# Optimization experiments

Hardware: AMD Instinct MI355X
Metric: run time of the kernel (lower is better)

The kernel has to match this reference:

```python
import jax, jax.numpy as jnp
import numpy as np

MAX_LEN = 128
N_SYMBOLS = 32000
HIDDEN = 1024
BATCH = 32


def setup_inputs() -> dict:
    key = jax.random.key(0)
    ks = jax.random.split(key, 8)
    s = 0.05  # weight scale for numerical stability
    return {
        "h": jax.random.normal(ks[0], (BATCH, HIDDEN), jnp.float32),
        "w_ih": jax.random.normal(ks[1], (3 * HIDDEN, HIDDEN), jnp.float32) * s,
        "w_hh": jax.random.normal(ks[2], (3 * HIDDEN, HIDDEN), jnp.float32) * s,
        "b_ih": jax.random.normal(ks[3], (3 * HIDDEN,), jnp.float32) * s,
        "b_hh": jax.random.normal(ks[4], (3 * HIDDEN,), jnp.float32) * s,
        "cls_w": jax.random.normal(ks[5], (N_SYMBOLS, HIDDEN), jnp.float32) * s,
        "cls_b": jax.random.normal(ks[6], (N_SYMBOLS,), jnp.float32) * s,
        "emb": jax.random.normal(ks[7], (N_SYMBOLS + 1, HIDDEN), jnp.float32),
    }


def reference(h, w_ih, w_hh, b_ih, b_hh, cls_w, cls_b, emb):
    B = h.shape[0]
    # BOS token embedding (row n_symbols), broadcast over batch.
    x0 = jnp.broadcast_to(emb[N_SYMBOLS], (B, HIDDEN))

    def step(carry, _):
        x, hs = carry
        gi = x @ w_ih.T + b_ih      # [B, 3H]
        gh = hs @ w_hh.T + b_hh     # [B, 3H]
        i_r, i_z, i_n = jnp.split(gi, 3, axis=-1)
        h_r, h_z, h_n = jnp.split(gh, 3, axis=-1)
        r = jax.nn.sigmoid(i_r + h_r)
        z = jax.nn.sigmoid(i_z + h_z)
        n = jnp.tanh(i_n + r * h_n)
        h_new = (1.0 - z) * n + z * hs
        logits = h_new @ cls_w.T + cls_b            # [B, V]
        tok = jnp.argmax(logits, axis=-1)            # [B]
        x_new = emb[tok]                             # [B, H]
        return (x_new, h_new), logits

    (_, _), logits = jax.lax.scan(step, (x0, h), None, length=MAX_LEN)
    # [max_len, B, n_symbols] == torch's cat(dim=-2).transpose(0, 1)
    return logits
```

## Files before the change

kernel.cpp:

```cpp
#include <hip/hip_runtime.h>
#include <math.h>

#define MAX_LEN 128
#define NSYM    32000
#define HID     1024
#define BATCH   32


__device__ __forceinline__ unsigned fkey(float x) {
    unsigned u = __float_as_uint(x);
    return (u & 0x80000000u) ? ~u : (u | 0x80000000u);
}

__global__ void init_slots(unsigned long long* slots) {
    int i = blockIdx.x * blockDim.x + threadIdx.x;
    if (i < MAX_LEN * BATCH) slots[i] = 0ULL;
}

__global__ __launch_bounds__(256) void gru_step(
    const float* __restrict__ h_in,
    const float* __restrict__ w_ih,
    const float* __restrict__ w_hh,
    const float* __restrict__ b_ih,
    const float* __restrict__ b_hh,
    const float* __restrict__ emb,
    const float* __restrict__ h_prev,
    float* __restrict__ h_next,
    const unsigned long long* __restrict__ slot_prev,
    int t)
{
    __shared__ float a_t[2][BATCH][129];
    __shared__ float w_t[24][128];
    __shared__ float s_gh[128][3];
    __shared__ int   s_tok[BATCH];

    const int tid  = threadIdx.x;
    const int pair = tid & 127;
    const int half = tid >> 7;
    const int b    = pair & 31;
    const int jj   = pair >> 5;
    const int j0   = blockIdx.x * 4;

    if (tid < BATCH) {
        int tok;
        if (t == 0) tok = NSYM;
        else {
            unsigned long long s = slot_prev[tid];
            tok = (int)(0xFFFFFFFFu - (unsigned)(s & 0xFFFFFFFFull));
        }
        s_tok[tid] = tok;
    }
    __syncthreads();

    const float* hp = (t == 0) ? h_in : h_prev;

    float acc0 = 0.f, acc1 = 0.f, acc2 = 0.f;

    float4 pw[3], pa[8];

    {
        const int k0 = 0;
        #pragma unroll
        for (int i = 0; i < 3; ++i) {
            int f = tid + 256 * i;
            int r = f >> 5, kq = f & 31;
            int rh = r / 12, rem = r % 12, g = rem >> 2, jx = rem & 3;
            const float* wsrc = rh ? w_hh : w_ih;
            size_t row = (size_t)(j0 + jx + 1024 * g);
            pw[i] = *(const float4*)&wsrc[row * HID + k0 + 4 * kq];
        }
        #pragma unroll
        for (int i = 0; i < 8; ++i) {
            int f = tid + 256 * i;
            int hh = f >> 10, bb = (f >> 5) & 31, kq = f & 31;
            const float* src = (hh == 0) ? &emb[(size_t)s_tok[bb] * HID]
                                         : &hp[(size_t)bb * HID];
            pa[i] = *(const float4*)&src[k0 + 4 * kq];
        }
    }

    const float* ar = &a_t[half][b][0];
    const float* w0 = &w_t[half * 12 + 0 + jj][0];
    const float* w1 = &w_t[half * 12 + 4 + jj][0];
    const float* w2 = &w_t[half * 12 + 8 + jj][0];

    for (int c = 0; c < 8; ++c) {
        __syncthreads();
        #pragma unroll
        for (int i = 0; i < 3; ++i) {
            int f = tid + 256 * i;
            int r = f >> 5, kq = f & 31;
            *(float4*)&w_t[r][4 * kq] = pw[i];
        }
        #pragma unroll
        for (int i = 0; i < 8; ++i) {
            int f = tid + 256 * i;
            int hh = f >> 10, bb = (f >> 5) & 31, kq = f & 31;
            float* dst = &a_t[hh][bb][4 * kq];
            dst[0] = pa[i].x; dst[1] = pa[i].y; dst[2] = pa[i].z; dst[3] = pa[i].w;
        }
        __syncthreads();

        if (c + 1 < 8) {
            const int k0 = (c + 1) * 128;
            #pragma unroll
            for (int i = 0; i < 3; ++i) {
                int f = tid + 256 * i;
                int r = f >> 5, kq = f & 31;
                int rh = r / 12, rem = r % 12, g = rem >> 2, jx = rem & 3;
                const float* wsrc = rh ? w_hh : w_ih;
                size_t row = (size_t)(j0 + jx + 1024 * g);
                pw[i] = *(const float4*)&wsrc[row * HID + k0 + 4 * kq];
            }
            #pragma unroll
            for (int i = 0; i < 8; ++i) {
                int f = tid + 256 * i;
                int hh = f >> 10, bb = (f >> 5) & 31, kq = f & 31;
                const float* src = (hh == 0) ? &emb[(size_t)s_tok[bb] * HID]
                                             : &hp[(size_t)bb * HID];
                pa[i] = *(const float4*)&src[k0 + 4 * kq];
            }
        }

        #pragma unroll 16
        for (int kk = 0; kk < 128; ++kk) {
            float av = ar[kk];
            acc0 = fmaf(av, w0[kk], acc0);
            acc1 = fmaf(av, w1[kk], acc1);
            acc2 = fmaf(av, w2[kk], acc2);
        }
    }

    __syncthreads();
    if (half == 1) {
        s_gh[pair][0] = acc0; s_gh[pair][1] = acc1; s_gh[pair][2] = acc2;
    }
    __syncthreads();
    if (half == 0) {
        int j = j0 + jj;
        float gir = acc0 + b_ih[j];
        float giz = acc1 + b_ih[j + 1024];
        float gin = acc2 + b_ih[j + 2048];
        float ghr = s_gh[pair][0] + b_hh[j];
        float ghz = s_gh[pair][1] + b_hh[j + 1024];
        float ghn = s_gh[pair][2] + b_hh[j + 2048];
        float r = 1.f / (1.f + expf(-(gir + ghr)));
        float z = 1.f / (1.f + expf(-(giz + ghz)));
        float n = tanhf(gin + r * ghn);
        float hv = hp[(size_t)b * HID + j];
        h_next[(size_t)b * HID + j] = (1.f - z) * n + z * hv;
    }
}

__global__ __launch_bounds__(256) void cls_step(
    const float* __restrict__ h_cur,
    const float* __restrict__ cls_w,
    const float* __restrict__ cls_b,
    float* __restrict__ out_t,
    unsigned long long* __restrict__ slot_t)
{
    __shared__ float w_t[128][65];
    __shared__ float a_t[BATCH][65];
    __shared__ unsigned long long s_best[BATCH];

    const int tid = threadIdx.x;
    const int tx  = tid & 31;
    const int ty  = tid >> 5;
    const int v0  = blockIdx.x * 128;

    if (tid < BATCH) s_best[tid] = 0ULL;

    float acc[4][4];
    #pragma unroll
    for (int i = 0; i < 4; ++i)
        #pragma unroll
        for (int m = 0; m < 4; ++m) acc[i][m] = 0.f;

    float4 pw[8], pa[2];

    {
        const int k0 = 0;
        #pragma unroll
        for (int i = 0; i < 8; ++i) {
            int f = tid + 256 * i;
            int v = f >> 4, kq = f & 15;
            pw[i] = *(const float4*)&cls_w[(size_t)(v0 + v) * HID + k0 + 4 * kq];
        }
        #pragma unroll
        for (int i = 0; i < 2; ++i) {
            int f = tid + 256 * i;
            int bb = f >> 4, kq = f & 15;
            pa[i] = *(const float4*)&h_cur[(size_t)bb * HID + k0 + 4 * kq];
        }
    }

    for (int c = 0; c < 16; ++c) {
        __syncthreads();
        #pragma unroll
        for (int i = 0; i < 8; ++i) {
            int f = tid + 256 * i;
            int v = f >> 4, kq = f & 15;
            float* dst = &w_t[v][4 * kq];
            dst[0] = pw[i].x; dst[1] = pw[i].y; dst[2] = pw[i].z; dst[3] = pw[i].w;
        }
        #pragma unroll
        for (int i = 0; i < 2; ++i) {
            int f = tid + 256 * i;
            int bb = f >> 4, kq = f & 15;
            float* dst = &a_t[bb][4 * kq];
            dst[0] = pa[i].x; dst[1] = pa[i].y; dst[2] = pa[i].z; dst[3] = pa[i].w;
        }
        __syncthreads();

        if (c + 1 < 16) {
            const int k0 = (c + 1) * 64;
            #pragma unroll
            for (int i = 0; i < 8; ++i) {
                int f = tid + 256 * i;
                int v = f >> 4, kq = f & 15;
                pw[i] = *(const float4*)&cls_w[(size_t)(v0 + v) * HID + k0 + 4 * kq];
            }
            #pragma unroll
            for (int i = 0; i < 2; ++i) {
                int f = tid + 256 * i;
                int bb = f >> 4, kq = f & 15;
                pa[i] = *(const float4*)&h_cur[(size_t)bb * HID + k0 + 4 * kq];
            }
        }

        #pragma unroll 8
        for (int kk = 0; kk < 64; ++kk) {
            float av[4], wv[4];
            #pragma unroll
            for (int i = 0; i < 4; ++i) av[i] = a_t[4 * ty + i][kk];
            #pragma unroll
            for (int m = 0; m < 4; ++m) wv[m] = w_t[tx + 32 * m][kk];
            #pragma unroll
            for (int i = 0; i < 4; ++i)
                #pragma unroll
                for (int m = 0; m < 4; ++m)
                    acc[i][m] = fmaf(av[i], wv[m], acc[i][m]);
        }
    }

    float cb[4];
    #pragma unroll
    for (int m = 0; m < 4; ++m) cb[m] = cls_b[v0 + tx + 32 * m];

    #pragma unroll
    for (int i = 0; i < 4; ++i) {
        int b = 4 * ty + i;
        unsigned long long best = 0ULL;
        #pragma unroll
        for (int m = 0; m < 4; ++m) {
            int v = v0 + tx + 32 * m;
            float val = acc[i][m] + cb[m];
            out_t[(size_t)b * NSYM + v] = val;
            unsigned long long pk =
                ((unsigned long long)fkey(val) << 32) |
                (unsigned long long)(0xFFFFFFFFu - (unsigned)v);
            if (pk > best) best = pk;
        }
        atomicMax(&s_best[b], best);
    }
    __syncthreads();
    if (tid < BATCH) atomicMax(&slot_t[tid], s_best[tid]);
}

extern "C" void kernel_launch(void* const* d_in, const int* in_sizes, int n_in,
                              void* d_out, int out_size, void* d_ws, size_t ws_size,
                              hipStream_t stream) {
    const float* h0    = (const float*)d_in[0];
    const float* w_ih  = (const float*)d_in[1];
    const float* w_hh  = (const float*)d_in[2];
    const float* b_ih  = (const float*)d_in[3];
    const float* b_hh  = (const float*)d_in[4];
    const float* cls_w = (const float*)d_in[5];
    const float* cls_b = (const float*)d_in[6];
    const float* emb   = (const float*)d_in[7];
    float* out = (float*)d_out;

    float* h_buf = (float*)d_ws;
    unsigned long long* slots =
        (unsigned long long*)((char*)d_ws + (size_t)2 * BATCH * HID * sizeof(float));

    init_slots<<<16, 256, 0, stream>>>(slots);

    for (int t = 0; t < MAX_LEN; ++t) {
        float* h_prev = h_buf + (size_t)((t + 1) & 1) * BATCH * HID;
        float* h_next = h_buf + (size_t)(t & 1) * BATCH * HID;
        const unsigned long long* slot_prev = slots + (size_t)(t > 0 ? (t - 1) : 0) * BATCH;

        gru_step<<<256, 256, 0, stream>>>(h0, w_ih, w_hh, b_ih, b_hh, emb,
                                          h_prev, h_next, slot_prev, t);
        cls_step<<<250, 256, 0, stream>>>(h_next, cls_w, cls_b,
                                          out + (size_t)t * BATCH * NSYM,
                                          slots + (size_t)t * BATCH);
    }
}
```

Measured before the change: 13.25 ms.

## Swizzle LDS tiles for float4 reads and stage logits for coalesced stores

Both GRU and classifier kernels replace padded shared-memory tiles with XOR-swizzled layouts, so inner loops can use float4 LDS reads without bank conflicts. The classifier thread mapping changes to a 2x8 register tile, and logits are transposed through shared memory so global stores go out as coalesced float4 writes. Launch bounds add a minimum of one block per CU. The aim is fewer LDS instructions, fewer bank conflicts and wider output stores. The cost is extra syncs and a shared-memory transpose in the epilogue.

```diff
diff --git a/kernel.cpp b/kernel.cpp
--- a/kernel.cpp
+++ b/kernel.cpp
@@ -17,7 +17,7 @@
     if (i < MAX_LEN * BATCH) slots[i] = 0ULL;
 }
 
-__global__ __launch_bounds__(256) void gru_step(
+__global__ __launch_bounds__(256, 1) void gru_step(
     const float* __restrict__ h_in,
     const float* __restrict__ w_ih,
     const float* __restrict__ w_hh,
@@ -29,24 +29,23 @@
     const unsigned long long* __restrict__ slot_prev,
     int t)
 {
-    __shared__ float a_t[2][BATCH][129];
     __shared__ float w_t[24][128];
+    __shared__ float a_t[2][32][128];
     __shared__ float s_gh[128][3];
     __shared__ int   s_tok[BATCH];
 
-    const int tid  = threadIdx.x;
-    const int pair = tid & 127;
-    const int half = tid >> 7;
-    const int b    = pair & 31;
-    const int jj   = pair >> 5;
-    const int j0   = blockIdx.x * 4;
+    const int tid = threadIdx.x;
+    const int b   = tid & 31;
+    const int j   = (tid >> 5) & 3;
+    const int s   = tid >> 7;
+    const int j0  = blockIdx.x * 4;
 
     if (tid < BATCH) {
         int tok;
         if (t == 0) tok = NSYM;
         else {
-            unsigned long long s = slot_prev[tid];
-            tok = (int)(0xFFFFFFFFu - (unsigned)(s & 0xFFFFFFFFull));
+            unsigned long long sl = slot_prev[tid];
+            tok = (int)(0xFFFFFFFFu - (unsigned)(sl & 0xFFFFFFFFull));
         }
         s_tok[tid] = tok;
     }
@@ -55,7 +54,6 @@
     const float* hp = (t == 0) ? h_in : h_prev;
 
     float acc0 = 0.f, acc1 = 0.f, acc2 = 0.f;
-
     float4 pw[3], pa[8];
 
     {
@@ -64,25 +62,24 @@
         for (int i = 0; i < 3; ++i) {
             int f = tid + 256 * i;
             int r = f >> 5, kq = f & 31;
-            int rh = r / 12, rem = r % 12, g = rem >> 2, jx = rem & 3;
-            const float* wsrc = rh ? w_hh : w_ih;
-            size_t row = (size_t)(j0 + jx + 1024 * g);
-            pw[i] = *(const float4*)&wsrc[row * HID + k0 + 4 * kq];
+            int rs = r / 12, rem = r % 12, g = rem >> 2, jx = rem & 3;
+            const float* wsrc = rs ? w_hh : w_ih;
+            pw[i] = *(const float4*)&wsrc[(size_t)(j0 + jx + 1024 * g) * HID + k0 + 4 * kq];
         }
         #pragma unroll
         for (int i = 0; i < 8; ++i) {
             int f = tid + 256 * i;
-            int hh = f >> 10, bb = (f >> 5) & 31, kq = f & 31;
-            const float* src = (hh == 0) ? &emb[(size_t)s_tok[bb] * HID]
-                                         : &hp[(size_t)bb * HID];
+            int ss = f >> 10, bb = (f >> 5) & 31, kq = f & 31;
+            const float* src = ss ? &hp[(size_t)bb * HID]
+                                  : &emb[(size_t)s_tok[bb] * HID];
             pa[i] = *(const float4*)&src[k0 + 4 * kq];
         }
     }
 
-    const float* ar = &a_t[half][b][0];
-    const float* w0 = &w_t[half * 12 + 0 + jj][0];
-    const float* w1 = &w_t[half * 12 + 4 + jj][0];
-    const float* w2 = &w_t[half * 12 + 8 + jj][0];
+    const float* wr0 = &w_t[12 * s + 0 + j][0];
+    const float* wr1 = &w_t[12 * s + 4 + j][0];
+    const float* wr2 = &w_t[12 * s + 8 + j][0];
+    const float* arow = &a_t[s][b][0];
 
     for (int c = 0; c < 8; ++c) {
         __syncthreads();
@@ -95,9 +92,8 @@
         #pragma unroll
         for (int i = 0; i < 8; ++i) {
             int f = tid + 256 * i;
-            int hh = f >> 10, bb = (f >> 5) & 31, kq = f & 31;
-            float* dst = &a_t[hh][bb][4 * kq];
-            dst[0] = pa[i].x; dst[1] = pa[i].y; dst[2] = pa[i].z; dst[3] = pa[i].w;
+            int ss = f >> 10, bb = (f >> 5) & 31, kq = f & 31;
+            *(float4*)&a_t[ss][bb][4 * (kq ^ bb)] = pa[i];
         }
         __syncthreads();
 
@@ -107,74 +103,81 @@
             for (int i = 0; i < 3; ++i) {
                 int f = tid + 256 * i;
                 int r = f >> 5, kq = f & 31;
-                int rh = r / 12, rem = r % 12, g = rem >> 2, jx = rem & 3;
-                const float* wsrc = rh ? w_hh : w_ih;
-                size_t row = (size_t)(j0 + jx + 1024 * g);
-                pw[i] = *(const float4*)&wsrc[row * HID + k0 + 4 * kq];
+                int rs = r / 12, rem = r % 12, g = rem >> 2, jx = rem & 3;
+                const float* wsrc = rs ? w_hh : w_ih;
+                pw[i] = *(const float4*)&wsrc[(size_t)(j0 + jx + 1024 * g) * HID + k0 + 4 * kq];
             }
             #pragma unroll
             for (int i = 0; i < 8; ++i) {
                 int f = tid + 256 * i;
-                int hh = f >> 10, bb = (f >> 5) & 31, kq = f & 31;
-                const float* src = (hh == 0) ? &emb[(size_t)s_tok[bb] * HID]
-                                             : &hp[(size_t)bb * HID];
+                int ss = f >> 10, bb = (f >> 5) & 31, kq = f & 31;
+                const float* src = ss ? &hp[(size_t)bb * HID]
+                                      : &emb[(size_t)s_tok[bb] * HID];
                 pa[i] = *(const float4*)&src[k0 + 4 * kq];
             }
         }
 
-        #pragma unroll 16
-        for (int kk = 0; kk < 128; ++kk) {
-            float av = ar[kk];
-            acc0 = fmaf(av, w0[kk], acc0);
-            acc1 = fmaf(av, w1[kk], acc1);
-            acc2 = fmaf(av, w2[kk], acc2);
-        }
-    }
-
-    __syncthreads();
-    if (half == 1) {
+        #pragma unroll 8
+        for (int q = 0; q < 32; ++q) {
+            float4 av = *(const float4*)&arow[4 * (q ^ b)];
+            float4 w0 = *(const float4*)&wr0[4 * q];
+            float4 w1 = *(const float4*)&wr1[4 * q];
+            float4 w2 = *(const float4*)&wr2[4 * q];
+            acc0 = fmaf(av.x, w0.x, acc0); acc0 = fmaf(av.y, w0.y, acc0);
+            acc0 = fmaf(av.z, w0.z, acc0); acc0 = fmaf(av.w, w0.w, acc0);
+            acc1 = fmaf(av.x, w1.x, acc1); acc1 = fmaf(av.y, w1.y, acc1);
+            acc1 = fmaf(av.z, w1.z, acc1); acc1 = fmaf(av.w, w1.w, acc1);
+            acc2 = fmaf(av.x, w2.x, acc2); acc2 = fmaf(av.y, w2.y, acc2);
+            acc2 = fmaf(av.z, w2.z, acc2); acc2 = fmaf(av.w, w2.w, acc2);
+        }
+    }
+
+    __syncthreads();
+    if (s == 1) {
+        int pair = tid & 127;
         s_gh[pair][0] = acc0; s_gh[pair][1] = acc1; s_gh[pair][2] = acc2;
     }
     __syncthreads();
-    if (half == 0) {
-        int j = j0 + jj;
-        float gir = acc0 + b_ih[j];
-        float giz = acc1 + b_ih[j + 1024];
-        float gin = acc2 + b_ih[j + 2048];
-        float ghr = s_gh[pair][0] + b_hh[j];
-        float ghz = s_gh[pair][1] + b_hh[j + 1024];
-        float ghn = s_gh[pair][2] + b_hh[j + 2048];
+    if (s == 0) {
+        int pair = tid & 127;
+        int jg = j0 + j;
+        float gir = acc0 + b_ih[jg];
+        float giz = acc1 + b_ih[jg + 1024];
+        float gin = acc2 + b_ih[jg + 2048];
+        float ghr = s_gh[pair][0] + b_hh[jg];
+        float ghz = s_gh[pair][1] + b_hh[jg + 1024];
+        float ghn = s_gh[pair][2] + b_hh[jg + 2048];
         float r = 1.f / (1.f + expf(-(gir + ghr)));
         float z = 1.f / (1.f + expf(-(giz + ghz)));
         float n = tanhf(gin + r * ghn);
-        float hv = hp[(size_t)b * HID + j];
-        h_next[(size_t)b * HID + j] = (1.f - z) * n + z * hv;
-    }
-}
-
-__global__ __launch_bounds__(256) void cls_step(
+        float hv = hp[(size_t)b * HID + jg];
+        h_next[(size_t)b * HID + jg] = (1.f - z) * n + z * hv;
+    }
+}
+
+__global__ __launch_bounds__(256, 1) void cls_step(
     const float* __restrict__ h_cur,
     const float* __restrict__ cls_w,
     const float* __restrict__ cls_b,
     float* __restrict__ out_t,
     unsigned long long* __restrict__ slot_t)
 {
-    __shared__ float w_t[128][65];
-    __shared__ float a_t[BATCH][65];
+    __shared__ float w_t[128][64];
+    __shared__ float a_t[32][64];
     __shared__ unsigned long long s_best[BATCH];
 
     const int tid = threadIdx.x;
-    const int tx  = tid & 31;
-    const int ty  = tid >> 5;
+    const int bq  = tid & 15;
+    const int vg  = tid >> 4;
     const int v0  = blockIdx.x * 128;
 
     if (tid < BATCH) s_best[tid] = 0ULL;
 
-    float acc[4][4];
+    float acc[2][8];
     #pragma unroll
-    for (int i = 0; i < 4; ++i)
-        #pragma unroll
-        for (int m = 0; m < 4; ++m) acc[i][m] = 0.f;
+    for (int h = 0; h < 2; ++h)
+        #pragma unroll
+        for (int i = 0; i < 8; ++i) acc[h][i] = 0.f;
 
     float4 pw[8], pa[2];
 
@@ -200,15 +203,13 @@
         for (int i = 0; i < 8; ++i) {
             int f = tid + 256 * i;
             int v = f >> 4, kq = f & 15;
-            float* dst = &w_t[v][4 * kq];
-            dst[0] = pw[i].x; dst[1] = pw[i].y; dst[2] = pw[i].z; dst[3] = pw[i].w;
+            *(float4*)&w_t[v][4 * (kq ^ (v & 15))] = pw[i];
         }
         #pragma unroll
         for (int i = 0; i < 2; ++i) {
             int f = tid + 256 * i;
             int bb = f >> 4, kq = f & 15;
-            float* dst = &a_t[bb][4 * kq];
-            dst[0] = pa[i].x; dst[1] = pa[i].y; dst[2] = pa[i].z; dst[3] = pa[i].w;
+            *(float4*)&a_t[bb][4 * (kq ^ (bb & 15))] = pa[i];
         }
         __syncthreads();
 
@@ -228,42 +229,59 @@
             }
         }
 
-        #pragma unroll 8
-        for (int kk = 0; kk < 64; ++kk) {
-            float av[4], wv[4];
-            #pragma unroll
-            for (int i = 0; i < 4; ++i) av[i] = a_t[4 * ty + i][kk];
-            #pragma unroll
-            for (int m = 0; m < 4; ++m) wv[m] = w_t[tx + 32 * m][kk];
-            #pragma unroll
-            for (int i = 0; i < 4; ++i)
-                #pragma unroll
-                for (int m = 0; m < 4; ++m)
-                    acc[i][m] = fmaf(av[i], wv[m], acc[i][m]);
-        }
-    }
-
-    float cb[4];
+        #pragma unroll 4
+        for (int q = 0; q < 16; ++q) {
+            float4 a0 = *(const float4*)&a_t[bq][4 * (q ^ bq)];
+            float4 a1 = *(const float4*)&a_t[bq + 16][4 * (q ^ bq)];
+            #pragma unroll
+            for (int i = 0; i < 8; ++i) {
+                float4 wv = *(const float4*)&w_t[vg + 16 * i][4 * (q ^ vg)];
+                acc[0][i] = fmaf(a0.x, wv.x, acc[0][i]);
+                acc[0][i] = fmaf(a0.y, wv.y, acc[0][i]);
+                acc[0][i] = fmaf(a0.z, wv.z, acc[0][i]);
+                acc[0][i] = fmaf(a0.w, wv.w, acc[0][i]);
+                acc[1][i] = fmaf(a1.x, wv.x, acc[1][i]);
+                acc[1][i] = fmaf(a1.y, wv.y, acc[1][i]);
+                acc[1][i] = fmaf(a1.z, wv.z, acc[1][i]);
+                acc[1][i] = fmaf(a1.w, wv.w, acc[1][i]);
+            }
+        }
+    }
+
+    float vals[2][8];
+    unsigned long long best0 = 0ULL, best1 = 0ULL;
     #pragma unroll
-    for (int m = 0; m < 4; ++m) cb[m] = cls_b[v0 + tx + 32 * m];
-
+    for (int i = 0; i < 8; ++i) {
+        int v = v0 + vg + 16 * i;
+        float cb = cls_b[v];
+        float x0 = acc[0][i] + cb;
+        float x1 = acc[1][i] + cb;
+        vals[0][i] = x0; vals[1][i] = x1;
+        unsigned long long p0 = ((unsigned long long)fkey(x0) << 32) |
+                                (unsigned long long)(0xFFFFFFFFu - (unsigned)v);
+        unsigned long long p1 = ((unsigned long long)fkey(x1) << 32) |
+                                (unsigned long long)(0xFFFFFFFFu - (unsigned)v);
+        if (p0 > best0) best0 = p0;
+        if (p1 > best1) best1 = p1;
+    }
+    atomicMax(&s_best[bq], best0);
+    atomicMax(&s_best[bq + 16], best1);
+
+    __syncthreads();
+    float* trans = &w_t[0][0];
     #pragma unroll
-    for (int i = 0; i < 4; ++i) {
-        int b = 4 * ty + i;
-        unsigned long long best = 0ULL;
-        #pragma unroll
-        for (int m = 0; m < 4; ++m) {
-            int v = v0 + tx + 32 * m;
-            float val = acc[i][m] + cb[m];
-            out_t[(size_t)b * NSYM + v] = val;
-            unsigned long long pk =
-                ((unsigned long long)fkey(val) << 32) |
-                (unsigned long long)(0xFFFFFFFFu - (unsigned)v);
-            if (pk > best) best = pk;
-        }
-        atomicMax(&s_best[b], best);
-    }
-    __syncthreads();
+    for (int i = 0; i < 8; ++i) {
+        trans[bq * 132 + vg + 16 * i]        = vals[0][i];
+        trans[(bq + 16) * 132 + vg + 16 * i] = vals[1][i];
+    }
+    __syncthreads();
+    #pragma unroll
+    for (int it = 0; it < 4; ++it) {
+        int idx = tid + 256 * it;
+        int v4 = idx & 31, bb = idx >> 5;
+        float4 o = *(const float4*)&trans[bb * 132 + 4 * v4];
+        *(float4*)&out_t[(size_t)bb * NSYM + v0 + 4 * v4] = o;
+    }
     if (tid < BATCH) atomicMax(&slot_t[tid], s_best[tid]);
 }
 
```

Measured after the change: 21.03 ms. +58.7%, slower.
